# Optimization experiments

Measured on AMD Instinct MI355X. Metric: run time of the kernel, lower is better.

The kernel has to match this reference:

```python
import jax, jax.numpy as jnp
import numpy as np

N_EMBD = 2560
N_HEAD = 32
HEAD_DIM = N_EMBD // N_HEAD  # 80
ROTARY_DIM = 32
SEQ = 2048
BSZ = 1


def _rope_tables(seq_len, rotary_dim, base=10000.0):
    inv_freq = 1.0 / (base ** (np.arange(0, rotary_dim, 2, dtype=np.float32) / rotary_dim))
    t = np.arange(seq_len, dtype=np.float32)
    freqs = np.outer(t, inv_freq)                      # [S, rd/2]
    emb = np.concatenate([freqs, freqs], axis=-1)      # [S, rd]
    return jnp.asarray(np.cos(emb)), jnp.asarray(np.sin(emb))


def setup_inputs() -> dict:
    key = jax.random.key(0)
    k1, k2, k3, k4, k5 = jax.random.split(key, 5)
    op_size = HEAD_DIM * (N_HEAD + 2 * N_HEAD)  # fused q,k,v => 3*n_embd
    hidden_states = jax.random.normal(k1, (BSZ, SEQ, N_EMBD), dtype=jnp.float32)
    Wqkv_w = jax.random.normal(k2, (op_size, N_EMBD), dtype=jnp.float32) * 0.02
    Wqkv_b = jax.random.normal(k3, (op_size,), dtype=jnp.float32) * 0.02
    out_w = jax.random.normal(k4, (N_EMBD, N_EMBD), dtype=jnp.float32) * 0.02
    out_b = jax.random.normal(k5, (N_EMBD,), dtype=jnp.float32) * 0.02
    cos, sin = _rope_tables(SEQ, ROTARY_DIM)
    return {"hidden_states": hidden_states, "Wqkv_w": Wqkv_w, "Wqkv_b": Wqkv_b,
            "out_w": out_w, "out_b": out_b, "cos": cos, "sin": sin}


def apply_partial_rotary(x, cos, sin):
    # x: [S, B, H, D]; cos/sin: [S, rd]
    rd = cos.shape[-1]
    c = cos[:, None, None, :]
    s = sin[:, None, None, :]
    x_rot = x[..., :rd]
    # NOTE: faithful to source -- rotated half is concatenated WITHOUT negation
    tmp = jnp.concatenate([x[..., rd // 2:rd], x[..., :rd // 2]], axis=-1)
    rotten = x_rot * c + tmp * s
    return jnp.concatenate([rotten, x[..., rd:]], axis=-1)


def reference(hidden_states, Wqkv_w, Wqkv_b, out_w, out_b, cos, sin):
    bsz, q_len, _ = hidden_states.shape
    qkv = hidden_states @ Wqkv_w.T + Wqkv_b            # [B, S, 3*E]
    q, k, v = jnp.split(qkv, 3, axis=-1)
    # [B, S, H, D] -> [S, B, H, D] for rotary
    q = q.reshape(bsz, q_len, N_HEAD, HEAD_DIM).transpose(1, 0, 2, 3)
    k = k.reshape(bsz, q_len, N_HEAD, HEAD_DIM).transpose(1, 0, 2, 3)
    v = v.reshape(bsz, q_len, N_HEAD, HEAD_DIM).transpose(0, 2, 1, 3)  # [B, H, S, D]
    cos_t, sin_t = cos[:q_len], sin[:q_len]
    q = apply_partial_rotary(q, cos_t, sin_t).transpose(1, 2, 0, 3)    # [B, H, S, D]
    k = apply_partial_rotary(k, cos_t, sin_t).transpose(1, 2, 0, 3)    # [B, H, S, D]
    scale = 1.0 / jnp.sqrt(jnp.asarray(HEAD_DIM, dtype=q.dtype))
    scores = jnp.einsum('bhqd,bhkd->bhqk', q, k) * scale
    causal = jnp.tril(jnp.ones((q_len, q_len), dtype=bool))
    scores = jnp.where(causal, scores, jnp.asarray(-1e30, dtype=scores.dtype))
    probs = jax.nn.softmax(scores, axis=-1)
    out = jnp.einsum('bhqk,bhkd->bhqd', probs, v)       # [B, H, S, D]
    out = out.transpose(0, 2, 1, 3).reshape(bsz, q_len, N_EMBD)
    return out @ out_w.T + out_b
```

## Files before the change

kernel.cpp:

```cpp
#include <hip/hip_runtime.h>
#include <cstdint>
#include <cstddef>

typedef unsigned short bf16_t;
typedef __attribute__((ext_vector_type(8))) short bf16x8;
typedef __attribute__((ext_vector_type(4))) float f32x4;

__device__ __forceinline__ float bf2f(bf16_t b) {
  unsigned int u = ((unsigned int)b) << 16;
  return __builtin_bit_cast(float, u);
}
__device__ __forceinline__ bf16_t f2bf(float f) {
  unsigned int u = __builtin_bit_cast(unsigned int, f);
  u += 0x7fffu + ((u >> 16) & 1u);
  return (bf16_t)(u >> 16);
}

constexpr int SEQ = 2048, NE = 2560, NH = 32, HD = 80, OP = 7680;

__global__ void cvt3(const float* __restrict__ s0, const float* __restrict__ s1,
                     const float* __restrict__ s2, bf16_t* __restrict__ d0,
                     bf16_t* __restrict__ d1, bf16_t* __restrict__ d2)
{
  constexpr int N0 = SEQ * NE / 4, N1 = OP * NE / 4;
  int t = blockIdx.x * 256 + threadIdx.x;
  const float* s; bf16_t* d;
  if (t < N0)            { s = s0; d = d0; }
  else if (t < N0 + N1)  { s = s1; d = d1; t -= N0; }
  else                   { s = s2; d = d2; t -= N0 + N1; }
  float4 v = ((const float4*)s)[t];
  ushort4 o;
  o.x = f2bf(v.x); o.y = f2bf(v.y); o.z = f2bf(v.z); o.w = f2bf(v.w);
  ((ushort4*)d)[t] = o;
}

__device__ __forceinline__ void store_out(bf16_t* p, float v) { *p = f2bf(v); }
__device__ __forceinline__ void store_out(float* p, float v)  { *p = v; }

template <typename OutT>
__global__ __launch_bounds__(256, 2) void gemm_bt_bias(
    const bf16_t* __restrict__ A,
    const bf16_t* __restrict__ B,
    const float*  __restrict__ bias,
    OutT* __restrict__ C,
    int M, int N, int K, int klen)
{
  __shared__ bf16_t As[2][128 * 32];
  __shared__ bf16_t Bs[2][128 * 32];

  const int tid  = threadIdx.x;
  const int lane = tid & 63;
  const int wave = tid >> 6;
  const int m0 = blockIdx.y * 128;
  const int n0 = blockIdx.x * 128;
  const int kbeg = blockIdx.z * klen;
  OutT* Cz = C + (size_t)blockIdx.z * M * N;
  const int mw = (wave >> 1) * 64;
  const int nw = (wave & 1) * 64;
  const int lm = lane & 15;
  const int lq = lane >> 4;

  f32x4 acc[4][4];
#pragma unroll
  for (int i = 0; i < 4; ++i)
#pragma unroll
    for (int j = 0; j < 4; ++j)
      acc[i][j] = (f32x4){0.f, 0.f, 0.f, 0.f};

  const int ldr = lane >> 2;
  const int ldc = (lane & 3) * 8;

  for (int kt = kbeg; kt < kbeg + klen; kt += 64) {
#pragma unroll
    for (int sub = 0; sub < 2; ++sub) {
#pragma unroll
      for (int r = 0; r < 2; ++r) {
        const int seg = wave * 2 + r;
        const int row = seg * 16 + ldr;
        const int col = kt + sub * 32 + ldc;
        const bf16_t* ga = A + (size_t)(m0 + row) * K + col;
        const bf16_t* gb = B + (size_t)(n0 + row) * K + col;
        __builtin_amdgcn_global_load_lds(
            (const __attribute__((address_space(1))) unsigned int*)ga,
            (__attribute__((address_space(3))) unsigned int*)&As[sub][seg * 512], 16, 0, 0);
        __builtin_amdgcn_global_load_lds(
            (const __attribute__((address_space(1))) unsigned int*)gb,
            (__attribute__((address_space(3))) unsigned int*)&Bs[sub][seg * 512], 16, 0, 0);
      }
    }
    __syncthreads();

#pragma unroll
    for (int sub = 0; sub < 2; ++sub) {
      bf16x8 af[4], bfq[4];
#pragma unroll
      for (int i = 0; i < 4; ++i)
        af[i] = *(const bf16x8*)&As[sub][(mw + i * 16 + lm) * 32 + lq * 8];
#pragma unroll
      for (int j = 0; j < 4; ++j)
        bfq[j] = *(const bf16x8*)&Bs[sub][(nw + j * 16 + lm) * 32 + lq * 8];

#pragma unroll
      for (int i = 0; i < 4; ++i)
#pragma unroll
        for (int j = 0; j < 4; ++j)
          acc[i][j] = __builtin_amdgcn_mfma_f32_16x16x32_bf16(af[i], bfq[j], acc[i][j], 0, 0, 0);
    }

    __syncthreads();
  }

#pragma unroll
  for (int i = 0; i < 4; ++i) {
#pragma unroll
    for (int j = 0; j < 4; ++j) {
      const int n = n0 + nw + j * 16 + lm;
      const float bv = bias ? bias[n] : 0.f;
#pragma unroll
      for (int r = 0; r < 4; ++r) {
        const int m = m0 + mw + i * 16 + lq * 4 + r;
        store_out(&Cz[(size_t)m * N + n], acc[i][j][r] + bv);
      }
    }
  }
}

__global__ void reduce2_bias(const float* __restrict__ p, const float* __restrict__ bias,
                             float* __restrict__ out)
{
  const int t = blockIdx.x * 256 + threadIdx.x;
  const float4 a = ((const float4*)p)[t];
  const float4 b = ((const float4*)(p + (size_t)SEQ * NE))[t];
  const float4 bv = ((const float4*)bias)[t % (NE / 4)];
  float4 r;
  r.x = a.x + b.x + bv.x; r.y = a.y + b.y + bv.y;
  r.z = a.z + b.z + bv.z; r.w = a.w + b.w + bv.w;
  ((float4*)out)[t] = r;
}

__global__ void rope_kernel(bf16_t* __restrict__ qkv,
                            const float* __restrict__ cosb,
                            const float* __restrict__ sinb)
{
  const int t = blockIdx.x * 256 + threadIdx.x;
  const int i  = t & 15;
  const int qk = (t >> 4) & 1;
  const int h  = (t >> 5) & 31;
  const int s  = t >> 10;
  const size_t base = (size_t)s * OP + qk * NE + h * HD;
  const float xi = bf2f(qkv[base + i]);
  const float xj = bf2f(qkv[base + i + 16]);
  const float c1 = cosb[s * 32 + i];
  const float s1 = sinb[s * 32 + i];
  const float c2 = cosb[s * 32 + i + 16];
  const float s2 = sinb[s * 32 + i + 16];
  qkv[base + i]      = f2bf(xi * c1 + xj * s1);
  qkv[base + i + 16] = f2bf(xj * c2 + xi * s2);
}

constexpr int KSTR = 96;
constexpr int VSTR = 72;
constexpr int PSTR = 72;

__global__ __launch_bounds__(256, 4) void attn_mfma(
    const bf16_t* __restrict__ qkv, bf16_t* __restrict__ aout)
{
  __shared__ bf16_t Ks[64 * KSTR];
  __shared__ bf16_t Vt[80 * VSTR];
  __shared__ bf16_t Ps[4][16 * PSTR];

  const int h    = blockIdx.y;
  const int qt   = (int)gridDim.x - 1 - blockIdx.x;
  const int q0   = qt * 64;
  const int tid  = threadIdx.x;
  const int lane = tid & 63;
  const int wave = tid >> 6;
  const int lm   = lane & 15;
  const int quad = lane >> 4;

  const int qg = q0 + 16 * wave + lm;

  const int koff = NE + h * HD;
  const int voff = 2 * NE + h * HD;
  const float SC = 0.1118033988749895f;

  bf16x8 qf[3];
  {
    const bf16_t* q_r = qkv + (size_t)qg * OP + h * HD;
#pragma unroll
    for (int ks = 0; ks < 3; ++ks) {
      const int col = ks * 32 + quad * 8;
      if (col < 80) qf[ks] = *(const bf16x8*)(q_r + col);
      else          qf[ks] = (bf16x8){0,0,0,0,0,0,0,0};
    }
  }

  int kofs[3];
#pragma unroll
  for (int r = 0; r < 3; ++r) {
    const int e = (wave * 3 + r) * 512 + lane * 8;
    const int row = e / 96, c = e % 96;
    kofs[r] = row * OP + (c < 80 ? c : c - 16);
  }

  const int vp = tid & 31;
  const int vg = tid >> 5;

  f32x4 oacc[5];
#pragma unroll
  for (int mt = 0; mt < 5; ++mt) oacc[mt] = (f32x4){0.f,0.f,0.f,0.f};
  float lsum = 0.f;

  const int ntiles = qt + 1;
  for (int t = 0; t < ntiles; ++t) {
    const int kb = t * 64;

#pragma unroll
    for (int r = 0; r < 3; ++r) {
      const bf16_t* g = qkv + (size_t)kb * OP + koff + kofs[r];
      __builtin_amdgcn_global_load_lds(
          (const __attribute__((address_space(1))) unsigned int*)g,
          (__attribute__((address_space(3))) unsigned int*)&Ks[(wave * 3 + r) * 512],
          16, 0, 0);
    }
    {
      const bf16_t* va = qkv + (size_t)(kb + 2 * vp) * OP + voff + vg * 10;
      const bf16_t* vb = va + OP;
      unsigned int wa[5], wb[5];
#pragma unroll
      for (int j = 0; j < 5; ++j) {
        wa[j] = *(const unsigned int*)(va + 2 * j);
        wb[j] = *(const unsigned int*)(vb + 2 * j);
      }
#pragma unroll
      for (int tt = 0; tt < 10; ++tt) {
        const unsigned int A = wa[tt >> 1], B = wb[tt >> 1];
        const unsigned int pk = (tt & 1) ? ((A >> 16) | (B & 0xffff0000u))
                                         : ((A & 0xffffu) | (B << 16));
        *(unsigned int*)&Vt[(vg * 10 + tt) * VSTR + 2 * vp] = pk;
      }
    }
    __syncthreads();

    f32x4 sacc[4];
#pragma unroll
    for (int mt = 0; mt < 4; ++mt) sacc[mt] = (f32x4){0.f,0.f,0.f,0.f};
#pragma unroll
    for (int ks = 0; ks < 3; ++ks) {
      bf16x8 kf[4];
#pragma unroll
      for (int mt = 0; mt < 4; ++mt)
        kf[mt] = *(const bf16x8*)&Ks[(mt * 16 + lm) * KSTR + ks * 32 + quad * 8];
#pragma unroll
      for (int mt = 0; mt < 4; ++mt)
        sacc[mt] = __builtin_amdgcn_mfma_f32_16x16x32_bf16(kf[mt], qf[ks], sacc[mt], 0, 0, 0);
    }

    const int keyb = kb + quad * 4;
#pragma unroll
    for (int mt = 0; mt < 4; ++mt) {
      float ps[4];
#pragma unroll
      for (int r = 0; r < 4; ++r) {
        float p = __expf(sacc[mt][r] * SC);
        p = (keyb + mt * 16 + r > qg) ? 0.f : p;
        ps[r] = p;
      }
      lsum += (ps[0] + ps[1]) + (ps[2] + ps[3]);
      ushort4 pk;
      pk.x = f2bf(ps[0]); pk.y = f2bf(ps[1]); pk.z = f2bf(ps[2]); pk.w = f2bf(ps[3]);
      *(ushort4*)&Ps[wave][lm * PSTR + mt * 16 + quad * 4] = pk;
    }

#pragma unroll
    for (int ks = 0; ks < 2; ++ks) {
      bf16x8 vf[5], pf;
#pragma unroll
      for (int mt = 0; mt < 5; ++mt)
        vf[mt] = *(const bf16x8*)&Vt[(mt * 16 + lm) * VSTR + ks * 32 + quad * 8];
      pf = *(const bf16x8*)&Ps[wave][lm * PSTR + ks * 32 + quad * 8];
#pragma unroll
      for (int mt = 0; mt < 5; ++mt)
        oacc[mt] = __builtin_amdgcn_mfma_f32_16x16x32_bf16(vf[mt], pf, oacc[mt], 0, 0, 0);
    }
    __syncthreads();
  }

  lsum += __shfl_xor(lsum, 16);
  lsum += __shfl_xor(lsum, 32);
  const float inv = 1.f / lsum;
  bf16_t* base = aout + (size_t)qg * NE + h * HD + quad * 4;
#pragma unroll
  for (int mt = 0; mt < 5; ++mt) {
    ushort4 st;
    st.x = f2bf(oacc[mt][0] * inv);
    st.y = f2bf(oacc[mt][1] * inv);
    st.z = f2bf(oacc[mt][2] * inv);
    st.w = f2bf(oacc[mt][3] * inv);
    *(ushort4*)(base + mt * 16) = st;
  }
}

extern "C" void kernel_launch(void* const* d_in, const int* in_sizes, int n_in,
                              void* d_out, int out_size, void* d_ws, size_t ws_size,
                              hipStream_t stream)
{
  const float* hs   = (const float*)d_in[0];
  const float* wqkv = (const float*)d_in[1];
  const float* bqkv = (const float*)d_in[2];
  const float* wout = (const float*)d_in[3];
  const float* bout = (const float*)d_in[4];
  const float* cosb = (const float*)d_in[5];
  const float* sinb = (const float*)d_in[6];

  bf16_t* hs_bf   = (bf16_t*)d_ws;
  bf16_t* wqkv_bf = hs_bf   + (size_t)SEQ * NE;
  bf16_t* wout_bf = wqkv_bf + (size_t)OP * NE;
  bf16_t* qkv     = wout_bf + (size_t)NE * NE;
  bf16_t* aout    = qkv     + (size_t)SEQ * OP;
  float*  out     = (float*)d_out;
  float*  pbuf    = (float*)d_ws;

  constexpr int CVT_T = (SEQ * NE + OP * NE + NE * NE) / 4;
  cvt3<<<CVT_T / 256, 256, 0, stream>>>(hs, wqkv, wout, hs_bf, wqkv_bf, wout_bf);

  gemm_bt_bias<bf16_t><<<dim3(OP / 128, SEQ / 128, 1), 256, 0, stream>>>(
      hs_bf, wqkv_bf, bqkv, qkv, SEQ, OP, NE, NE);
  rope_kernel<<<(SEQ * NH * 2 * 16) / 256, 256, 0, stream>>>(qkv, cosb, sinb);
  attn_mfma<<<dim3(SEQ / 64, NH), 256, 0, stream>>>(qkv, aout);
  gemm_bt_bias<float><<<dim3(NE / 128, SEQ / 128, 2), 256, 0, stream>>>(
      aout, wout_bf, nullptr, pbuf, SEQ, NE, NE, NE / 2);
  reduce2_bias<<<(SEQ * NE / 4) / 256, 256, 0, stream>>>(pbuf, bout, out);
}
```

Baseline: 432.1 us.

## Pre-transpose V into global buffer and async-load it; mask only the diagonal tile

A new kernel transposes V per head into a [H, D, S] buffer that reuses the hidden-state workspace. The attention kernel can then fill its V tile with async global-to-LDS loads, the same way it loads K, instead of doing a register shuffle transpose on every tile. The causal mask check now runs only on the last (diagonal) tile, and exp is computed with a hardware exp2 using a folded log2e scale. This adds an extra kernel launch and one extra pass over V through memory.

```diff
diff --git a/kernel.cpp b/kernel.cpp
--- a/kernel.cpp
+++ b/kernel.cpp
@@ -14,6 +14,9 @@
   unsigned int u = __builtin_bit_cast(unsigned int, f);
   u += 0x7fffu + ((u >> 16) & 1u);
   return (bf16_t)(u >> 16);
+}
+__device__ __forceinline__ float exp2_hw(float x) {
+  return __builtin_amdgcn_exp2f(x);
 }
 
 constexpr int SEQ = 2048, NE = 2560, NH = 32, HD = 80, OP = 7680;
@@ -158,15 +161,45 @@
   qkv[base + i + 16] = f2bf(xj * c2 + xi * s2);
 }
 
+constexpr int TSTR = 82;
+__global__ void vtrans(const bf16_t* __restrict__ qkv, bf16_t* __restrict__ vtg)
+{
+  __shared__ bf16_t T[64 * TSTR];
+  const int h  = blockIdx.y;
+  const int sb = blockIdx.x * 64;
+  const int tid = threadIdx.x;
+  const int voff = 2 * NE + h * HD;
+
+#pragma unroll
+  for (int i = 0; i < 10; ++i) {
+    const int u = i * 256 + tid;
+    const int row = u / 40, c = u % 40;
+    const unsigned int w = *(const unsigned int*)(qkv + (size_t)(sb + row) * OP + voff + 2 * c);
+    *(unsigned int*)&T[row * TSTR + 2 * c] = w;
+  }
+  __syncthreads();
+
+  bf16_t* vh = vtg + (size_t)h * HD * SEQ;
+#pragma unroll
+  for (int i = 0; i < 10; ++i) {
+    const int u = i * 256 + tid;
+    const int d = u >> 5, sp = u & 31;
+    const unsigned int lo = T[(2 * sp) * TSTR + d];
+    const unsigned int hi = T[(2 * sp + 1) * TSTR + d];
+    *(unsigned int*)(vh + (size_t)d * SEQ + sb + 2 * sp) = lo | (hi << 16);
+  }
+}
+
 constexpr int KSTR = 96;
 constexpr int VSTR = 72;
 constexpr int PSTR = 72;
 
 __global__ __launch_bounds__(256, 4) void attn_mfma(
-    const bf16_t* __restrict__ qkv, bf16_t* __restrict__ aout)
-{
-  __shared__ bf16_t Ks[64 * KSTR];
-  __shared__ bf16_t Vt[80 * VSTR];
+    const bf16_t* __restrict__ qkv, const bf16_t* __restrict__ vtg,
+    bf16_t* __restrict__ aout)
+{
+  __shared__ bf16_t Ks[12 * 512];
+  __shared__ bf16_t Vt[12 * 512];
   __shared__ bf16_t Ps[4][16 * PSTR];
 
   const int h    = blockIdx.y;
@@ -181,8 +214,8 @@
   const int qg = q0 + 16 * wave + lm;
 
   const int koff = NE + h * HD;
-  const int voff = 2 * NE + h * HD;
-  const float SC = 0.1118033988749895f;
+  const bf16_t* vh = vtg + (size_t)h * HD * SEQ;
+  const float EC = 0.1118033988749895f * 1.4426950408889634f;
 
   bf16x8 qf[3];
   {
@@ -202,9 +235,15 @@
     const int row = e / 96, c = e % 96;
     kofs[r] = row * OP + (c < 80 ? c : c - 16);
   }
-
-  const int vp = tid & 31;
-  const int vg = tid >> 5;
+  int vofs[3];
+#pragma unroll
+  for (int r = 0; r < 3; ++r) {
+    const int e = (wave * 3 + r) * 512 + lane * 8;
+    int row = e / 72;
+    const int c = e % 72;
+    if (row >= 80) row -= 80;
+    vofs[r] = row * SEQ + (c < 64 ? c : c - 16);
+  }
 
   f32x4 oacc[5];
 #pragma unroll
@@ -217,28 +256,16 @@
 
 #pragma unroll
     for (int r = 0; r < 3; ++r) {
-      const bf16_t* g = qkv + (size_t)kb * OP + koff + kofs[r];
+      const bf16_t* gk = qkv + (size_t)kb * OP + koff + kofs[r];
       __builtin_amdgcn_global_load_lds(
-          (const __attribute__((address_space(1))) unsigned int*)g,
+          (const __attribute__((address_space(1))) unsigned int*)gk,
           (__attribute__((address_space(3))) unsigned int*)&Ks[(wave * 3 + r) * 512],
           16, 0, 0);
-    }
-    {
-      const bf16_t* va = qkv + (size_t)(kb + 2 * vp) * OP + voff + vg * 10;
-      const bf16_t* vb = va + OP;
-      unsigned int wa[5], wb[5];
-#pragma unroll
-      for (int j = 0; j < 5; ++j) {
-        wa[j] = *(const unsigned int*)(va + 2 * j);
-        wb[j] = *(const unsigned int*)(vb + 2 * j);
-      }
-#pragma unroll
-      for (int tt = 0; tt < 10; ++tt) {
-        const unsigned int A = wa[tt >> 1], B = wb[tt >> 1];
-        const unsigned int pk = (tt & 1) ? ((A >> 16) | (B & 0xffff0000u))
-                                         : ((A & 0xffffu) | (B << 16));
-        *(unsigned int*)&Vt[(vg * 10 + tt) * VSTR + 2 * vp] = pk;
-      }
+      const bf16_t* gv = vh + kb + vofs[r];
+      __builtin_amdgcn_global_load_lds(
+          (const __attribute__((address_space(1))) unsigned int*)gv,
+          (__attribute__((address_space(3))) unsigned int*)&Vt[(wave * 3 + r) * 512],
+          16, 0, 0);
     }
     __syncthreads();
 
@@ -256,20 +283,33 @@
         sacc[mt] = __builtin_amdgcn_mfma_f32_16x16x32_bf16(kf[mt], qf[ks], sacc[mt], 0, 0, 0);
     }
 
-    const int keyb = kb + quad * 4;
-#pragma unroll
-    for (int mt = 0; mt < 4; ++mt) {
-      float ps[4];
-#pragma unroll
-      for (int r = 0; r < 4; ++r) {
-        float p = __expf(sacc[mt][r] * SC);
-        p = (keyb + mt * 16 + r > qg) ? 0.f : p;
-        ps[r] = p;
+    if (t == ntiles - 1) {
+      const int keyb = kb + quad * 4;
+#pragma unroll
+      for (int mt = 0; mt < 4; ++mt) {
+        float ps[4];
+#pragma unroll
+        for (int r = 0; r < 4; ++r) {
+          float p = exp2_hw(sacc[mt][r] * EC);
+          p = (keyb + mt * 16 + r > qg) ? 0.f : p;
+          ps[r] = p;
+        }
+        lsum += (ps[0] + ps[1]) + (ps[2] + ps[3]);
+        ushort4 pk;
+        pk.x = f2bf(ps[0]); pk.y = f2bf(ps[1]); pk.z = f2bf(ps[2]); pk.w = f2bf(ps[3]);
+        *(ushort4*)&Ps[wave][lm * PSTR + mt * 16 + quad * 4] = pk;
       }
-      lsum += (ps[0] + ps[1]) + (ps[2] + ps[3]);
-      ushort4 pk;
-      pk.x = f2bf(ps[0]); pk.y = f2bf(ps[1]); pk.z = f2bf(ps[2]); pk.w = f2bf(ps[3]);
-      *(ushort4*)&Ps[wave][lm * PSTR + mt * 16 + quad * 4] = pk;
+    } else {
+#pragma unroll
+      for (int mt = 0; mt < 4; ++mt) {
+        float ps[4];
+#pragma unroll
+        for (int r = 0; r < 4; ++r) ps[r] = exp2_hw(sacc[mt][r] * EC);
+        lsum += (ps[0] + ps[1]) + (ps[2] + ps[3]);
+        ushort4 pk;
+        pk.x = f2bf(ps[0]); pk.y = f2bf(ps[1]); pk.z = f2bf(ps[2]); pk.w = f2bf(ps[3]);
+        *(ushort4*)&Ps[wave][lm * PSTR + mt * 16 + quad * 4] = pk;
+      }
     }
 
 #pragma unroll
@@ -319,6 +359,7 @@
   bf16_t* qkv     = wout_bf + (size_t)NE * NE;
   bf16_t* aout    = qkv     + (size_t)SEQ * OP;
   float*  out     = (float*)d_out;
+  bf16_t* vtg     = hs_bf;
   float*  pbuf    = (float*)d_ws;
 
   constexpr int CVT_T = (SEQ * NE + OP * NE + NE * NE) / 4;
@@ -327,7 +368,8 @@
   gemm_bt_bias<bf16_t><<<dim3(OP / 128, SEQ / 128, 1), 256, 0, stream>>>(
       hs_bf, wqkv_bf, bqkv, qkv, SEQ, OP, NE, NE);
   rope_kernel<<<(SEQ * NH * 2 * 16) / 256, 256, 0, stream>>>(qkv, cosb, sinb);
-  attn_mfma<<<dim3(SEQ / 64, NH), 256, 0, stream>>>(qkv, aout);
+  vtrans<<<dim3(SEQ / 64, NH), 256, 0, stream>>>(qkv, vtg);
+  attn_mfma<<<dim3(SEQ / 64, NH), 256, 0, stream>>>(qkv, vtg, aout);
   gemm_bt_bias<float><<<dim3(NE / 128, SEQ / 128, 2), 256, 0, stream>>>(
       aout, wout_bf, nullptr, pbuf, SEQ, NE, NE, NE / 2);
   reduce2_bias<<<(SEQ * NE / 4) / 256, 256, 0, stream>>>(pbuf, bout, out);
```

Result: faster. 415.0 us (-3.9%).
